# Kernel optimization log

Measured on AMD Instinct MI355X. Metric: run time of the kernel, lower is better.

Reference implementation:

```python
import jax, jax.numpy as jnp
import numpy as np

EPS = 1e-6

def _quant_per_token(x):
    # dynamic per-token symmetric int8 quantization (simulated in float)
    s = jnp.max(jnp.abs(x), axis=-1, keepdims=True) / 127.0  # [T,1]
    q = jnp.clip(jnp.round(x / s), -127.0, 127.0)
    return q, s

def _quant_weight(W):
    # per-output-channel symmetric int8 weight quantization (W: [out,in])
    s = jnp.max(jnp.abs(W), axis=1, keepdims=True) / 127.0  # [out,1]
    q = jnp.round(W / s)
    return q, s

def _w8a8(qx, sx, W, b):
    # int8xint8 GEMM with per-token act scale and per-channel weight scale, fp out
    qw, sw = _quant_weight(W)
    return (qx @ qw.T) * (sx * sw.T) + b

def _rmsnorm_bias(x, w, b, eps=EPS):
    # RMSNormGeneral: x * rsqrt(mean(x^2)+eps) * w + b (no mean subtraction)
    var = jnp.mean(x * x, axis=-1, keepdims=True)
    return x * jax.lax.rsqrt(var + eps) * w + b

def setup_inputs() -> dict:
    key = jax.random.key(0)
    ks = jax.random.split(key, 16)
    E, H, F = 1280, 20, 5120
    B, S = 16, 1024
    T = B * S
    d = {
        'hidden': jax.random.normal(ks[0], (T, E), jnp.float32),
        'ln1_w': jax.random.uniform(ks[1], (E,), jnp.float32, 0.5, 1.5),
        'ln1_b': jax.random.normal(ks[2], (E,), jnp.float32) * 0.02,
        'ln2_w': jax.random.uniform(ks[3], (E,), jnp.float32, 0.5, 1.5),
        'ln2_b': jax.random.normal(ks[4], (E,), jnp.float32) * 0.02,
        'W_qkv': jax.random.normal(ks[5], (3 * E, E), jnp.float32) * 0.02,
        'b_qkv': jax.random.normal(ks[6], (3 * E,), jnp.float32) * 0.02,
        'W_out': jax.random.normal(ks[7], (E, E), jnp.float32) * 0.02,
        'b_out': jax.random.normal(ks[8], (E,), jnp.float32) * 0.02,
        'W_fc1': jax.random.normal(ks[9], (F, E), jnp.float32) * 0.02,
        'b_fc1': jax.random.normal(ks[10], (F,), jnp.float32) * 0.02,
        'W_fc2': jax.random.normal(ks[11], (E, F), jnp.float32) * 0.02,
        'b_fc2': jax.random.normal(ks[12], (E,), jnp.float32) * 0.02,
        'bsz': B,
        'seqlen': S,
    }
    return d

def reference(hidden, ln1_w, ln1_b, ln2_w, ln2_b, W_qkv, b_qkv, W_out, b_out,
              W_fc1, b_fc1, W_fc2, b_fc2, bsz, seqlen):
    E = hidden.shape[-1]
    H = 20
    hd = E // H

    # --- self-attention block ---
    residual = hidden
    y = _rmsnorm_bias(hidden, ln1_w, ln1_b)
    qx, sx = _quant_per_token(y)
    qkv = _w8a8(qx, sx, W_qkv, b_qkv)                      # [T, 3E]
    q, k, v = jnp.split(qkv, 3, axis=-1)
    q = q.reshape(bsz, seqlen, H, hd)
    k = k.reshape(bsz, seqlen, H, hd)
    v = v.reshape(bsz, seqlen, H, hd)
    scale = 1.0 / np.sqrt(hd)
    scores = jnp.einsum('bqhd,bkhd->bhqk', q, k) * scale   # non-causal
    probs = jax.nn.softmax(scores, axis=-1)
    attn = jnp.einsum('bhqk,bkhd->bqhd', probs, v).reshape(bsz * seqlen, E)
    qa, sa = _quant_per_token(attn)
    o = _w8a8(qa, sa, W_out, b_out)
    hidden = residual + o

    # --- MLP block ---
    residual = hidden
    y = _rmsnorm_bias(hidden, ln2_w, ln2_b)
    qx, sx = _quant_per_token(y)
    f1 = _w8a8(qx, sx, W_fc1, b_fc1)                       # [T, F]
    g = jax.nn.gelu(f1, approximate=False)                 # fused gelu_and_quant
    qg, sg = _quant_per_token(g)
    f2 = _w8a8(qg, sg, W_fc2, b_fc2)
    return residual + f2
```

## Files before the change

### kernel.cpp

```cpp
#include <hip/hip_runtime.h>
#include <hip/hip_bf16.h>
#include <stdint.h>

#define E_DIM 1280
#define F_DIM 5120
#define T_DIM 16384
#define B_SZ  16
#define S_LEN 1024
#define NH    20

typedef int v4i __attribute__((ext_vector_type(4)));
typedef __attribute__((ext_vector_type(8))) short v8s;
typedef __attribute__((ext_vector_type(4))) float v4f;

__device__ __forceinline__ float wred_sum(float v) {
#pragma unroll
  for (int m = 32; m > 0; m >>= 1) v += __shfl_xor(v, m, 64);
  return v;
}
__device__ __forceinline__ float wred_max(float v) {
#pragma unroll
  for (int m = 32; m > 0; m >>= 1) v = fmaxf(v, __shfl_xor(v, m, 64));
  return v;
}
__device__ __forceinline__ void gload_lds16(const void* g, void* l) {
  __builtin_amdgcn_global_load_lds((const __attribute__((address_space(1))) void*)g,
                                   (__attribute__((address_space(3))) void*)l, 16, 0, 0);
}

__global__ __launch_bounds__(256) void wquant_kernel(
    const float* __restrict__ W, int8_t* __restrict__ qw, float* __restrict__ sw, int K) {
  __shared__ float red[4];
  const int row = blockIdx.x;
  const int tid = threadIdx.x;
  const float* wr = W + (size_t)row * K;
  float amax = 0.f;
  for (int c = tid; c < K; c += 256) amax = fmaxf(amax, fabsf(wr[c]));
  amax = wred_max(amax);
  if ((tid & 63) == 0) red[tid >> 6] = amax;
  __syncthreads();
  amax = fmaxf(fmaxf(red[0], red[1]), fmaxf(red[2], red[3]));
  float sc = amax * (1.0f / 127.0f);
  if (tid == 0) sw[row] = sc;
  for (int c = tid; c < K; c += 256) {
    float qv = rintf(wr[c] / sc);
    qw[(size_t)row * K + c] = (int8_t)qv;
  }
}

__global__ __launch_bounds__(256) void rms_quant_kernel(
    const float* __restrict__ x, const float* __restrict__ w, const float* __restrict__ b,
    int8_t* __restrict__ q, float* __restrict__ s) {
  __shared__ float red[4];
  const int row = blockIdx.x;
  const int tid = threadIdx.x;
  const float* xr = x + (size_t)row * E_DIM;
  float vals[5];
  float ss = 0.f;
#pragma unroll
  for (int i = 0; i < 5; ++i) {
    float v = xr[tid + i * 256];
    vals[i] = v; ss += v * v;
  }
  ss = wred_sum(ss);
  if ((tid & 63) == 0) red[tid >> 6] = ss;
  __syncthreads();
  ss = red[0] + red[1] + red[2] + red[3];
  float rstd = rsqrtf(ss * (1.0f / E_DIM) + 1e-6f);
  float y[5]; float amax = 0.f;
#pragma unroll
  for (int i = 0; i < 5; ++i) {
    int c = tid + i * 256;
    float v = vals[i] * rstd * w[c] + b[c];
    y[i] = v;
    amax = fmaxf(amax, fabsf(v));
  }
  amax = wred_max(amax);
  __syncthreads();
  if ((tid & 63) == 0) red[tid >> 6] = amax;
  __syncthreads();
  amax = fmaxf(fmaxf(red[0], red[1]), fmaxf(red[2], red[3]));
  float sc = amax * (1.0f / 127.0f);
  if (tid == 0) s[row] = sc;
#pragma unroll
  for (int i = 0; i < 5; ++i) {
    int c = tid + i * 256;
    float qv = rintf(y[i] / sc);
    qv = fminf(fmaxf(qv, -127.f), 127.f);
    q[(size_t)row * E_DIM + c] = (int8_t)qv;
  }
}

__global__ __launch_bounds__(256) void row_quant_bf_kernel(
    const __hip_bfloat16* __restrict__ x, int8_t* __restrict__ q, float* __restrict__ s) {
  __shared__ float red[4];
  const int row = blockIdx.x;
  const int tid = threadIdx.x;
  const __hip_bfloat16* xr = x + (size_t)row * E_DIM;
  float vals[5]; float amax = 0.f;
#pragma unroll
  for (int i = 0; i < 5; ++i) {
    float v = __bfloat162float(xr[tid + i * 256]);
    vals[i] = v;
    amax = fmaxf(amax, fabsf(v));
  }
  amax = wred_max(amax);
  if ((tid & 63) == 0) red[tid >> 6] = amax;
  __syncthreads();
  amax = fmaxf(fmaxf(red[0], red[1]), fmaxf(red[2], red[3]));
  float sc = amax * (1.0f / 127.0f);
  if (tid == 0) s[row] = sc;
#pragma unroll
  for (int i = 0; i < 5; ++i) {
    int c = tid + i * 256;
    float qv = rintf(vals[i] / sc);
    qv = fminf(fmaxf(qv, -127.f), 127.f);
    q[(size_t)row * E_DIM + c] = (int8_t)qv;
  }
}

__global__ __launch_bounds__(256) void gelu_quant_kernel(
    const __hip_bfloat16* __restrict__ f1, int8_t* __restrict__ q, float* __restrict__ s) {
  __shared__ float red[4];
  const int row = blockIdx.x;
  const int tid = threadIdx.x;
  const __hip_bfloat16* xr = f1 + (size_t)row * F_DIM;
  float g[20]; float amax = 0.f;
#pragma unroll
  for (int i = 0; i < 20; ++i) {
    float v = __bfloat162float(xr[tid + i * 256]);
    float gv = 0.5f * v * (1.0f + erff(v * 0.70710678118654752440f));
    g[i] = gv;
    amax = fmaxf(amax, fabsf(gv));
  }
  amax = wred_max(amax);
  if ((tid & 63) == 0) red[tid >> 6] = amax;
  __syncthreads();
  amax = fmaxf(fmaxf(red[0], red[1]), fmaxf(red[2], red[3]));
  float sc = amax * (1.0f / 127.0f);
  if (tid == 0) s[row] = sc;
  int8_t* qr = q + (size_t)row * (2 * F_DIM);
#pragma unroll
  for (int i = 0; i < 20; ++i) {
    int c = tid + i * 256;
    float qv = rintf(g[i] / sc);
    qv = fminf(fmaxf(qv, -127.f), 127.f);
    qr[c] = (int8_t)qv;
  }
}

template <int MODE>
__global__ __launch_bounds__(512, 2) void gemm256_i8(
    const int8_t* __restrict__ A, const int8_t* __restrict__ B,
    const float* __restrict__ sx, const float* __restrict__ sw,
    const float* __restrict__ bias, const float* __restrict__ resid,
    void* __restrict__ outp, int M, int N, int K, int lda) {
  __shared__ __align__(16) int8_t As[2][2][256 * 64];
  __shared__ __align__(16) int8_t Bs[2][2][256 * 64];

  const int tid = threadIdx.x;
  const int lane = tid & 63;
  const int wave = tid >> 6;
  const int wm = wave >> 2;
  const int wn = wave & 3;
  const int l16 = lane & 15;
  const int quad = lane >> 4;
  const int choff = (quad ^ ((l16 >> 1) & 3)) << 4;

  const int nwg = gridDim.x;
  const int ntn = N >> 8;
  const int u = (blockIdx.x & 7) * (nwg >> 3) + (blockIdx.x >> 3);
  const int tm = u / ntn, tn = u % ntn;
  const int m0 = tm << 8, n0 = tn << 8;

  const int8_t* A_blk = A + (size_t)m0 * lda;
  const int8_t* B_blk = B + (size_t)n0 * K;

  const int r0 = tid >> 2;
  const int sch = ((tid & 3) ^ ((tid >> 3) & 3)) << 4;

#define STAGE_A(KT, DST)                                                         \
  {                                                                              \
    gload_lds16(A_blk + (size_t)r0 * lda + (size_t)(KT)*64 + sch,                \
                (DST) + tid * 16);                                               \
    gload_lds16(A_blk + (size_t)(r0 + 128) * lda + (size_t)(KT)*64 + sch,        \
                (DST) + 8192 + tid * 16);                                        \
  }
#define STAGE_B(KT, DST)                                                         \
  {                                                                              \
    gload_lds16(B_blk + (size_t)r0 * K + (size_t)(KT)*64 + sch,                  \
                (DST) + tid * 16);                                               \
    gload_lds16(B_blk + (size_t)(r0 + 128) * K + (size_t)(KT)*64 + sch,          \
                (DST) + 8192 + tid * 16);                                        \
  }

  v4i acc[8][4];
#pragma unroll
  for (int i = 0; i < 8; ++i)
#pragma unroll
    for (int j = 0; j < 4; ++j) acc[i][j] = (v4i){0, 0, 0, 0};

  const int nk = K >> 6;
  const int niter = nk >> 1;

  STAGE_A(0, &As[0][0][0]); STAGE_B(0, &Bs[0][0][0]);
  STAGE_A(1, &As[0][1][0]); STAGE_B(1, &Bs[0][1][0]);
  asm volatile("s_waitcnt vmcnt(4)" ::: "memory");
  asm volatile("s_barrier" ::: "memory");

#pragma unroll 1
  for (int i = 0; i < niter - 1; ++i) {
    const int pr = i & 1;
    const int kt2 = 2 * i + 2;
#pragma unroll
    for (int ph = 0; ph < 4; ++ph) {
      const int tt = ph >> 1;
      const int qm = ph & 1;
      const int8_t* At = &As[pr][tt][0];
      const int8_t* Bt = &Bs[pr][tt][0];
      v4i af[4], bf[4];
#pragma unroll
      for (int ii = 0; ii < 4; ++ii)
        af[ii] = *(const v4i*)(At + (wm * 128 + qm * 64 + ii * 16 + l16) * 64 + choff);
#pragma unroll
      for (int jj = 0; jj < 4; ++jj)
        bf[jj] = *(const v4i*)(Bt + (wn * 64 + jj * 16 + l16) * 64 + choff);
      if (qm == 0) {
        STAGE_A(kt2 + tt, &As[pr ^ 1][tt][0]);
      } else {
        STAGE_B(kt2 + tt, &Bs[pr ^ 1][tt][0]);
      }
      asm volatile("s_barrier" ::: "memory");
      __builtin_amdgcn_s_setprio(1);
#pragma unroll
      for (int ii = 0; ii < 4; ++ii)
#pragma unroll
        for (int jj = 0; jj < 4; ++jj)
          acc[qm * 4 + ii][jj] = __builtin_amdgcn_mfma_i32_16x16x64_i8(
              af[ii], bf[jj], acc[qm * 4 + ii][jj], 0, 0, 0);
      __builtin_amdgcn_s_setprio(0);
      if (qm == 1) asm volatile("s_waitcnt vmcnt(4)" ::: "memory");
      asm volatile("s_barrier" ::: "memory");
    }
  }

  {
    const int pr = (niter - 1) & 1;
#pragma unroll
    for (int ph = 0; ph < 4; ++ph) {
      const int tt = ph >> 1;
      const int qm = ph & 1;
      const int8_t* At = &As[pr][tt][0];
      const int8_t* Bt = &Bs[pr][tt][0];
      v4i af[4], bf[4];
#pragma unroll
      for (int ii = 0; ii < 4; ++ii)
        af[ii] = *(const v4i*)(At + (wm * 128 + qm * 64 + ii * 16 + l16) * 64 + choff);
#pragma unroll
      for (int jj = 0; jj < 4; ++jj)
        bf[jj] = *(const v4i*)(Bt + (wn * 64 + jj * 16 + l16) * 64 + choff);
      asm volatile("s_barrier" ::: "memory");
      __builtin_amdgcn_s_setprio(1);
#pragma unroll
      for (int ii = 0; ii < 4; ++ii)
#pragma unroll
        for (int jj = 0; jj < 4; ++jj)
          acc[qm * 4 + ii][jj] = __builtin_amdgcn_mfma_i32_16x16x64_i8(
              af[ii], bf[jj], acc[qm * 4 + ii][jj], 0, 0, 0);
      __builtin_amdgcn_s_setprio(0);
      if (ph == 1) asm volatile("s_waitcnt vmcnt(0)" ::: "memory");
      asm volatile("s_barrier" ::: "memory");
    }
  }
#undef STAGE_A
#undef STAGE_B

  float swv[4], bv[4];
#pragma unroll
  for (int jj = 0; jj < 4; ++jj) {
    int n = n0 + wn * 64 + jj * 16 + l16;
    swv[jj] = sw[n];
    bv[jj] = bias[n];
  }
#pragma unroll
  for (int mf = 0; mf < 8; ++mf) {
#pragma unroll
    for (int r = 0; r < 4; ++r) {
      int m = m0 + wm * 128 + mf * 16 + quad * 4 + r;
      float sxm = sx[m];
#pragma unroll
      for (int jj = 0; jj < 4; ++jj) {
        int n = n0 + wn * 64 + jj * 16 + l16;
        float v = (float)acc[mf][jj][r] * (sxm * swv[jj]) + bv[jj];
        if constexpr (MODE == 0) {
          ((__hip_bfloat16*)outp)[(size_t)m * N + n] = __float2bfloat16(v);
        } else {
          ((float*)outp)[(size_t)m * N + n] = v + resid[(size_t)m * N + n];
        }
      }
    }
  }
}

template <int MODE>
__global__ __launch_bounds__(256, 2) void gemm128_i8(
    const int8_t* __restrict__ A, const int8_t* __restrict__ B,
    const float* __restrict__ sx, const float* __restrict__ sw,
    const float* __restrict__ bias, const float* __restrict__ resid,
    void* __restrict__ outp, int M, int N, int K, int lda) {
  __shared__ __align__(16) int8_t As[4][128 * 64];
  __shared__ __align__(16) int8_t Bs[4][128 * 64];

  const int tid = threadIdx.x;
  const int lane = tid & 63;
  const int wave = tid >> 6;
  const int wm = wave >> 1;
  const int wn = wave & 1;
  const int l16 = lane & 15;
  const int quad = lane >> 4;
  const int choff = (quad ^ ((l16 >> 1) & 3)) << 4;

  const int nwg = gridDim.x;
  const int ntn = N >> 7;
  const int u = (blockIdx.x & 7) * (nwg >> 3) + (blockIdx.x >> 3);
  const int tm = u / ntn, tn = u % ntn;
  const int m0 = tm << 7, n0 = tn << 7;

  const int8_t* A_blk = A + (size_t)m0 * lda;
  const int8_t* B_blk = B + (size_t)n0 * K;

  const int r0 = tid >> 2;
  const int sch = ((tid & 3) ^ ((tid >> 3) & 3)) << 4;

#define STAGE_A(KT, SLOT)                                                        \
  {                                                                              \
    gload_lds16(A_blk + (size_t)r0 * lda + (size_t)(KT)*64 + sch,                \
                &As[SLOT][tid * 16]);                                            \
    gload_lds16(A_blk + (size_t)(r0 + 64) * lda + (size_t)(KT)*64 + sch,         \
                &As[SLOT][4096 + tid * 16]);                                     \
  }
#define STAGE_B(KT, SLOT)                                                        \
  {                                                                              \
    gload_lds16(B_blk + (size_t)r0 * K + (size_t)(KT)*64 + sch,                  \
                &Bs[SLOT][tid * 16]);                                            \
    gload_lds16(B_blk + (size_t)(r0 + 64) * K + (size_t)(KT)*64 + sch,           \
                &Bs[SLOT][4096 + tid * 16]);                                     \
  }

#define KTILE(SLOT, STAGE_STMT, WAIT_STMT)                                       \
  {                                                                              \
    const int8_t* At = &As[SLOT][0];                                             \
    const int8_t* Bt = &Bs[SLOT][0];                                             \
    v4i af[4], bf[4];                                                            \
    _Pragma("unroll") for (int ii = 0; ii < 4; ++ii)                             \
        af[ii] = *(const v4i*)(At + (wm * 64 + ii * 16 + l16) * 64 + choff);     \
    _Pragma("unroll") for (int jj = 0; jj < 4; ++jj)                             \
        bf[jj] = *(const v4i*)(Bt + (wn * 64 + jj * 16 + l16) * 64 + choff);     \
    STAGE_STMT;                                                                  \
    asm volatile("s_barrier" ::: "memory");                                      \
    __builtin_amdgcn_s_setprio(1);                                               \
    _Pragma("unroll") for (int ii = 0; ii < 4; ++ii)                             \
        _Pragma("unroll") for (int jj = 0; jj < 4; ++jj)                         \
            acc[ii][jj] = __builtin_amdgcn_mfma_i32_16x16x64_i8(                 \
                af[ii], bf[jj], acc[ii][jj], 0, 0, 0);                           \
    __builtin_amdgcn_s_setprio(0);                                               \
    WAIT_STMT;                                                                   \
    asm volatile("s_barrier" ::: "memory");                                      \
  }

  v4i acc[4][4];
#pragma unroll
  for (int i = 0; i < 4; ++i)
#pragma unroll
    for (int j = 0; j < 4; ++j) acc[i][j] = (v4i){0, 0, 0, 0};

  const int nk = K >> 6;

  STAGE_A(0, 0); STAGE_B(0, 0);
  STAGE_A(1, 1); STAGE_B(1, 1);
  STAGE_A(2, 2); STAGE_B(2, 2);
  asm volatile("s_waitcnt vmcnt(8)" ::: "memory");
  asm volatile("s_barrier" ::: "memory");

#pragma unroll 1
  for (int kt = 0; kt < nk - 3; ++kt) {
    const int sl = kt & 3;
    const int s3 = (kt + 3) & 3;
    KTILE(sl, { STAGE_A(kt + 3, s3); STAGE_B(kt + 3, s3); },
          asm volatile("s_waitcnt vmcnt(8)" ::: "memory"));
  }
  KTILE((nk - 3) & 3, ((void)0), asm volatile("s_waitcnt vmcnt(4)" ::: "memory"));
  KTILE((nk - 2) & 3, ((void)0), asm volatile("s_waitcnt vmcnt(0)" ::: "memory"));
  KTILE((nk - 1) & 3, ((void)0), ((void)0));
#undef KTILE
#undef STAGE_A
#undef STAGE_B

  float swv[4], bv[4];
#pragma unroll
  for (int jj = 0; jj < 4; ++jj) {
    int n = n0 + wn * 64 + jj * 16 + l16;
    swv[jj] = sw[n];
    bv[jj] = bias[n];
  }
#pragma unroll
  for (int ii = 0; ii < 4; ++ii) {
#pragma unroll
    for (int r = 0; r < 4; ++r) {
      int m = m0 + wm * 64 + ii * 16 + quad * 4 + r;
      float sxm = sx[m];
#pragma unroll
      for (int jj = 0; jj < 4; ++jj) {
        int n = n0 + wn * 64 + jj * 16 + l16;
        float v = (float)acc[ii][jj][r] * (sxm * swv[jj]) + bv[jj];
        if constexpr (MODE == 0) {
          ((__hip_bfloat16*)outp)[(size_t)m * N + n] = __float2bfloat16(v);
        } else {
          ((float*)outp)[(size_t)m * N + n] = v + resid[(size_t)m * N + n];
        }
      }
    }
  }
}

__global__ __launch_bounds__(256) void vt_kernel(
    const __hip_bfloat16* __restrict__ qkv, __hip_bfloat16* __restrict__ Vt) {
  __shared__ __hip_bfloat16 tile[64][72];
  const int bh = blockIdx.y, kc = blockIdx.x;
  const int b = bh / NH, h = bh % NH;
  const int tid = threadIdx.x;
  const size_t base = ((size_t)b * S_LEN + (size_t)kc * 64) * (3 * E_DIM) + 2 * E_DIM + h * 64;
#pragma unroll
  for (int i = 0; i < 2; ++i) {
    int idx = tid + i * 256;
    int row = idx >> 3, c8 = (idx & 7) * 8;
    *(uint4*)&tile[row][c8] = *(const uint4*)(qkv + base + (size_t)row * (3 * E_DIM) + c8);
  }
  __syncthreads();
#pragma unroll
  for (int i = 0; i < 2; ++i) {
    int idx = tid + i * 256;
    int d = idx >> 3, k8 = (idx & 7) * 8;
    __hip_bfloat16 v[8] __attribute__((aligned(16)));
#pragma unroll
    for (int j = 0; j < 8; ++j) v[j] = tile[k8 + j][d];
    *(uint4*)&Vt[((size_t)bh * 64 + d) * 1024 + (size_t)kc * 64 + k8] = *(uint4*)v;
  }
}

__global__ __launch_bounds__(256) void attn_flash_kernel(
    const __hip_bfloat16* __restrict__ qkv, const __hip_bfloat16* __restrict__ Vt,
    __hip_bfloat16* __restrict__ attn) {
  constexpr int E3 = 3 * E_DIM;
  __shared__ __align__(16) __hip_bfloat16 Ks[128 * 64];
  __shared__ __align__(16) __hip_bfloat16 Vs[64 * 128];
  __shared__ __align__(16) __hip_bfloat16 Ps[4][16 * 128];
  __shared__ float stats[4][16];

  const int tid = threadIdx.x;
  const int lane = tid & 63;
  const int wave = tid >> 6;
  const int l16 = lane & 15;
  const int quad = lane >> 4;
  const int wg = (blockIdx.x & 7) * 640 + (blockIdx.x >> 3);
  const int bh = wg >> 4;
  const int b = bh / NH, h = bh % NH;
  const int q0 = (wg & 15) * 64;
  const size_t base_t = (size_t)b * S_LEN;

  v8s qb0, qb1;
  {
    const __hip_bfloat16* qp =
        qkv + (base_t + q0 + wave * 16 + l16) * (size_t)E3 + h * 64 + quad * 8;
    qb0 = *(const v8s*)qp;
    qb1 = *(const v8s*)(qp + 32);
  }

  const __hip_bfloat16* kgbase = qkv + base_t * E3 + E_DIM + h * 64;
  const __hip_bfloat16* vgbase = Vt + (size_t)bh * 64 * 1024;
  __hip_bfloat16* pw = Ps[wave];

  const __hip_bfloat16* ksrc[4];
  const __hip_bfloat16* vsrc[4];
  int cdst[4];
#pragma unroll
  for (int i = 0; i < 4; ++i) {
    int c = tid + i * 256;
    cdst[i] = c * 16;
    int row = c >> 3, lc = c & 7;
    int gc = lc ^ (row & 7);
    ksrc[i] = kgbase + (size_t)row * E3 + gc * 8;
    int d = c >> 4, lcv = c & 15;
    int gv = lcv ^ (d & 15);
    vsrc[i] = vgbase + (size_t)d * 1024 + gv * 8;
  }

#pragma unroll
  for (int i = 0; i < 4; ++i) gload_lds16(ksrc[i], (char*)Ks + cdst[i]);
#pragma unroll
  for (int i = 0; i < 4; ++i) gload_lds16(vsrc[i], (char*)Vs + cdst[i]);
  __syncthreads();

  constexpr float CEXP = 0.18033688011112042f;
  float m_prev = -3.0e38f;
  float mc = m_prev * CEXP;
  float lsum = 0.f;
  v4f oc[4];
#pragma unroll
  for (int dt = 0; dt < 4; ++dt) oc[dt] = (v4f){0.f, 0.f, 0.f, 0.f};

#pragma unroll 1
  for (int t = 0; t < 8; ++t) {
    v4i kreg[4], vreg[4];
    if (t < 7) {
#pragma unroll
      for (int i = 0; i < 4; ++i)
        kreg[i] = *(const v4i*)(ksrc[i] + (size_t)(t + 1) * 128 * E3);
#pragma unroll
      for (int i = 0; i < 4; ++i)
        vreg[i] = *(const v4i*)(vsrc[i] + (size_t)(t + 1) * 128);
    }

    v4f accT[8];
    __builtin_amdgcn_s_setprio(1);
#pragma unroll
    for (int nt = 0; nt < 8; ++nt) {
      int row = nt * 16 + l16;
      const char* kr = (const char*)Ks + row * 128;
      v8s ak0 = *(const v8s*)(kr + ((quad ^ (row & 7)) * 16));
      v8s ak1 = *(const v8s*)(kr + (((quad + 4) ^ (row & 7)) * 16));
      v4f z = {0.f, 0.f, 0.f, 0.f};
      z = __builtin_amdgcn_mfma_f32_16x16x32_bf16(ak0, qb0, z, 0, 0, 0);
      accT[nt] = __builtin_amdgcn_mfma_f32_16x16x32_bf16(ak1, qb1, accT[nt] = z, 0, 0, 0);
    }
    __builtin_amdgcn_s_setprio(0);

    float mt = -3.0e38f;
#pragma unroll
    for (int nt = 0; nt < 8; ++nt)
      mt = fmaxf(mt, fmaxf(fmaxf(accT[nt][0], accT[nt][1]),
                           fmaxf(accT[nt][2], accT[nt][3])));
    mt = fmaxf(mt, __shfl_xor(mt, 16, 64));
    mt = fmaxf(mt, __shfl_xor(mt, 32, 64));
    if (__any(mt > m_prev + 48.0f)) {
      float m_new = fmaxf(m_prev, mt);
      float mcn = m_new * CEXP;
      float alpha = exp2f(m_prev * CEXP - mcn);
      m_prev = m_new;
      mc = mcn;
      lsum *= alpha;
      if (quad == 0) stats[wave][l16] = alpha;
      v4f a4 = *(v4f*)&stats[wave][quad * 4];
#pragma unroll
      for (int dt = 0; dt < 4; ++dt)
#pragma unroll
        for (int r = 0; r < 4; ++r) oc[dt][r] *= a4[r];
    }
    float ts = 0.f;
#pragma unroll
    for (int nt = 0; nt < 8; ++nt)
#pragma unroll
      for (int r = 0; r < 4; ++r) {
        float e = exp2f(fmaf(accT[nt][r], CEXP, -mc));
        accT[nt][r] = e;
        ts += e;
      }
    lsum += ts;
#pragma unroll
    for (int nt = 0; nt < 8; ++nt) {
      __hip_bfloat16 pk[4] __attribute__((aligned(8)));
#pragma unroll
      for (int r = 0; r < 4; ++r) pk[r] = __float2bfloat16(accT[nt][r]);
      int lcq = 2 * nt + (quad >> 1);
      *(uint2*)((char*)pw + l16 * 256 + ((lcq ^ l16) * 16) + (quad & 1) * 8) = *(uint2*)pk;
    }
    __builtin_amdgcn_s_setprio(1);
#pragma unroll
    for (int ks = 0; ks < 4; ++ks) {
      int pch = (ks * 4 + quad) ^ l16;
      v8s ap = *(const v8s*)((char*)pw + l16 * 256 + pch * 16);
#pragma unroll
      for (int dt = 0; dt < 4; ++dt) {
        int d = dt * 16 + l16;
        v8s bv = *(const v8s*)((char*)Vs + d * 256 + (((ks * 4 + quad) ^ l16) * 16));
        oc[dt] = __builtin_amdgcn_mfma_f32_16x16x32_bf16(ap, bv, oc[dt], 0, 0, 0);
      }
    }
    __builtin_amdgcn_s_setprio(0);

    __syncthreads();
    if (t < 7) {
#pragma unroll
      for (int i = 0; i < 4; ++i) *(v4i*)((char*)Ks + cdst[i]) = kreg[i];
#pragma unroll
      for (int i = 0; i < 4; ++i) *(v4i*)((char*)Vs + cdst[i]) = vreg[i];
    }
    __syncthreads();
  }

  lsum += __shfl_xor(lsum, 16, 64);
  lsum += __shfl_xor(lsum, 32, 64);
  if (quad == 0) stats[wave][l16] = lsum;
  v4f l4 = *(v4f*)&stats[wave][quad * 4];
  float inv[4];
#pragma unroll
  for (int r = 0; r < 4; ++r) inv[r] = 1.0f / l4[r];
#pragma unroll
  for (int dt = 0; dt < 4; ++dt)
#pragma unroll
    for (int r = 0; r < 4; ++r) {
      int tok = q0 + wave * 16 + quad * 4 + r;
      attn[(base_t + tok) * (size_t)E_DIM + h * 64 + dt * 16 + l16] =
          __float2bfloat16(oc[dt][r] * inv[r]);
    }
}

extern "C" void kernel_launch(void* const* d_in, const int* in_sizes, int n_in,
                              void* d_out, int out_size, void* d_ws, size_t ws_size,
                              hipStream_t stream) {
  const float* hidden = (const float*)d_in[0];
  const float* ln1_w = (const float*)d_in[1];
  const float* ln1_b = (const float*)d_in[2];
  const float* ln2_w = (const float*)d_in[3];
  const float* ln2_b = (const float*)d_in[4];
  const float* W_qkv = (const float*)d_in[5];
  const float* b_qkv = (const float*)d_in[6];
  const float* W_out = (const float*)d_in[7];
  const float* b_out = (const float*)d_in[8];
  const float* W_fc1 = (const float*)d_in[9];
  const float* b_fc1 = (const float*)d_in[10];
  const float* W_fc2 = (const float*)d_in[11];
  const float* b_fc2 = (const float*)d_in[12];

  char* ws = (char*)d_ws;
  size_t off = 0;
  auto alloc = [&](size_t bytes) {
    void* p = ws + off;
    off += (bytes + 255) & ~(size_t)255;
    return p;
  };
  int8_t* qw_qkv = (int8_t*)alloc((size_t)3 * E_DIM * E_DIM);
  int8_t* qw_out = (int8_t*)alloc((size_t)E_DIM * E_DIM);
  int8_t* qw_fc1 = (int8_t*)alloc((size_t)F_DIM * E_DIM);
  int8_t* qw_fc2 = (int8_t*)alloc((size_t)E_DIM * F_DIM);
  float* sw_qkv = (float*)alloc((size_t)3 * E_DIM * 4);
  float* sw_out = (float*)alloc((size_t)E_DIM * 4);
  float* sw_fc1 = (float*)alloc((size_t)F_DIM * 4);
  float* sw_fc2 = (float*)alloc((size_t)E_DIM * 4);
  float* sx1 = (float*)alloc((size_t)T_DIM * 4);
  float* sa  = (float*)alloc((size_t)T_DIM * 4);
  float* sx2 = (float*)alloc((size_t)T_DIM * 4);
  float* sg  = (float*)alloc((size_t)T_DIM * 4);
  int8_t* qx = (int8_t*)alloc((size_t)T_DIM * E_DIM);
  char* R = (char*)alloc((size_t)T_DIM * 3 * E_DIM * 2 +
                         (size_t)T_DIM * E_DIM * 4);
  __hip_bfloat16* qkv_bf = (__hip_bfloat16*)R;
  __hip_bfloat16* attn_bf = (__hip_bfloat16*)(R + (size_t)T_DIM * 3 * E_DIM * 2);
  __hip_bfloat16* Vt = (__hip_bfloat16*)(R + (size_t)T_DIM * 3 * E_DIM * 2 +
                                         (size_t)T_DIM * E_DIM * 2);
  __hip_bfloat16* f1_bf = (__hip_bfloat16*)R;
  int8_t* qg = (int8_t*)R;
  float* hidden2 = (float*)d_out;

  wquant_kernel<<<3 * E_DIM, 256, 0, stream>>>(W_qkv, qw_qkv, sw_qkv, E_DIM);
  wquant_kernel<<<E_DIM, 256, 0, stream>>>(W_out, qw_out, sw_out, E_DIM);
  wquant_kernel<<<F_DIM, 256, 0, stream>>>(W_fc1, qw_fc1, sw_fc1, E_DIM);
  wquant_kernel<<<E_DIM, 256, 0, stream>>>(W_fc2, qw_fc2, sw_fc2, F_DIM);
  rms_quant_kernel<<<T_DIM, 256, 0, stream>>>(hidden, ln1_w, ln1_b, qx, sx1);
  gemm256_i8<0><<<(T_DIM / 256) * (3 * E_DIM / 256), 512, 0, stream>>>(
      qx, qw_qkv, sx1, sw_qkv, b_qkv, nullptr, qkv_bf, T_DIM, 3 * E_DIM, E_DIM, E_DIM);
  vt_kernel<<<dim3(S_LEN / 64, B_SZ * NH), 256, 0, stream>>>(qkv_bf, Vt);
  attn_flash_kernel<<<(S_LEN / 64) * B_SZ * NH, 256, 0, stream>>>(qkv_bf, Vt, attn_bf);
  row_quant_bf_kernel<<<T_DIM, 256, 0, stream>>>(attn_bf, qx, sa);
  gemm128_i8<1><<<(T_DIM / 128) * (E_DIM / 128), 256, 0, stream>>>(
      qx, qw_out, sa, sw_out, b_out, hidden, hidden2, T_DIM, E_DIM, E_DIM, E_DIM);
  rms_quant_kernel<<<T_DIM, 256, 0, stream>>>(hidden2, ln2_w, ln2_b, qx, sx2);
  gemm256_i8<0><<<(T_DIM / 256) * (F_DIM / 256), 512, 0, stream>>>(
      qx, qw_fc1, sx2, sw_fc1, b_fc1, nullptr, f1_bf, T_DIM, F_DIM, E_DIM, E_DIM);
  gelu_quant_kernel<<<T_DIM, 256, 0, stream>>>(f1_bf, qg, sg);
  gemm128_i8<1><<<(T_DIM / 128) * (E_DIM / 128), 256, 0, stream>>>(
      qg, qw_fc2, sg, sw_fc2, b_fc2, hidden2, (float*)d_out, T_DIM, E_DIM, F_DIM, 2 * F_DIM);
}
```

Before: 1.045 ms.

## Drop register prefetch in flash attention, load K/V directly to LDS each tile

Removes the register-staged prefetch of the next K/V tile and instead issues direct global-to-LDS loads at the start of each iteration between barriers. It also precomputes the swizzled LDS offsets outside the loop and adds a launch bound of 3 blocks per CU. The aim is to cut VGPR pressure so more waves fit per CU and hide latency through occupancy. The cost is that loads are no longer overlapped with compute inside a block, so each tile now waits on memory latency.

```diff
diff --git a/kernel.cpp b/kernel.cpp
--- a/kernel.cpp
+++ b/kernel.cpp
@@ -448,7 +448,7 @@
   }
 }
 
-__global__ __launch_bounds__(256) void attn_flash_kernel(
+__global__ __launch_bounds__(256, 3) void attn_flash_kernel(
     const __hip_bfloat16* __restrict__ qkv, const __hip_bfloat16* __restrict__ Vt,
     __hip_bfloat16* __restrict__ attn) {
   constexpr int E3 = 3 * E_DIM;
@@ -476,30 +476,44 @@
     qb1 = *(const v8s*)(qp + 32);
   }
 
-  const __hip_bfloat16* kgbase = qkv + base_t * E3 + E_DIM + h * 64;
-  const __hip_bfloat16* vgbase = Vt + (size_t)bh * 64 * 1024;
   __hip_bfloat16* pw = Ps[wave];
 
-  const __hip_bfloat16* ksrc[4];
-  const __hip_bfloat16* vsrc[4];
+  const __hip_bfloat16* kp[4];
+  const __hip_bfloat16* vp[4];
   int cdst[4];
-#pragma unroll
-  for (int i = 0; i < 4; ++i) {
-    int c = tid + i * 256;
-    cdst[i] = c * 16;
-    int row = c >> 3, lc = c & 7;
-    int gc = lc ^ (row & 7);
-    ksrc[i] = kgbase + (size_t)row * E3 + gc * 8;
-    int d = c >> 4, lcv = c & 15;
-    int gv = lcv ^ (d & 15);
-    vsrc[i] = vgbase + (size_t)d * 1024 + gv * 8;
-  }
-
-#pragma unroll
-  for (int i = 0; i < 4; ++i) gload_lds16(ksrc[i], (char*)Ks + cdst[i]);
-#pragma unroll
-  for (int i = 0; i < 4; ++i) gload_lds16(vsrc[i], (char*)Vs + cdst[i]);
-  __syncthreads();
+  {
+    const __hip_bfloat16* kgbase = qkv + base_t * E3 + E_DIM + h * 64;
+    const __hip_bfloat16* vgbase = Vt + (size_t)bh * 64 * 1024;
+#pragma unroll
+    for (int i = 0; i < 4; ++i) {
+      int c = tid + i * 256;
+      cdst[i] = c * 16;
+      int row = c >> 3, lc = c & 7;
+      int gc = lc ^ (row & 7);
+      kp[i] = kgbase + (size_t)row * E3 + gc * 8;
+      int d = c >> 4, lcv = c & 15;
+      int gv = lcv ^ (d & 15);
+      vp[i] = vgbase + (size_t)d * 1024 + gv * 8;
+    }
+  }
+
+  const int cho0 = (quad ^ (l16 & 7)) << 4;
+  const int cho1 = ((quad + 4) ^ (l16 & 7)) << 4;
+  const char* krbase = (const char*)Ks + l16 * 128;
+  char* pwr[8];
+#pragma unroll
+  for (int nt = 0; nt < 8; ++nt) {
+    int lcq = 2 * nt + (quad >> 1);
+    pwr[nt] = (char*)pw + l16 * 256 + ((lcq ^ l16) * 16) + (quad & 1) * 8;
+  }
+  const char* pvp[4];
+  int vvo[4];
+#pragma unroll
+  for (int ks = 0; ks < 4; ++ks) {
+    int pch16 = (((ks * 4 + quad) ^ l16) << 4);
+    pvp[ks] = (char*)pw + l16 * 256 + pch16;
+    vvo[ks] = l16 * 256 + pch16;
+  }
 
   constexpr float CEXP = 0.18033688011112042f;
   float m_prev = -3.0e38f;
@@ -511,24 +525,22 @@
 
 #pragma unroll 1
   for (int t = 0; t < 8; ++t) {
-    v4i kreg[4], vreg[4];
-    if (t < 7) {
-#pragma unroll
-      for (int i = 0; i < 4; ++i)
-        kreg[i] = *(const v4i*)(ksrc[i] + (size_t)(t + 1) * 128 * E3);
-#pragma unroll
-      for (int i = 0; i < 4; ++i)
-        vreg[i] = *(const v4i*)(vsrc[i] + (size_t)(t + 1) * 128);
-    }
+    __syncthreads();
+#pragma unroll
+    for (int i = 0; i < 4; ++i) gload_lds16(kp[i], (char*)Ks + cdst[i]);
+#pragma unroll
+    for (int i = 0; i < 4; ++i) gload_lds16(vp[i], (char*)Vs + cdst[i]);
+#pragma unroll
+    for (int i = 0; i < 4; ++i) { kp[i] += (size_t)128 * E3; vp[i] += 128; }
+    __syncthreads();
 
     v4f accT[8];
     __builtin_amdgcn_s_setprio(1);
 #pragma unroll
     for (int nt = 0; nt < 8; ++nt) {
-      int row = nt * 16 + l16;
-      const char* kr = (const char*)Ks + row * 128;
-      v8s ak0 = *(const v8s*)(kr + ((quad ^ (row & 7)) * 16));
-      v8s ak1 = *(const v8s*)(kr + (((quad + 4) ^ (row & 7)) * 16));
+      const char* kr = krbase + nt * 2048;
+      v8s ak0 = *(const v8s*)(kr + cho0);
+      v8s ak1 = *(const v8s*)(kr + cho1);
       v4f z = {0.f, 0.f, 0.f, 0.f};
       z = __builtin_amdgcn_mfma_f32_16x16x32_bf16(ak0, qb0, z, 0, 0, 0);
       accT[nt] = __builtin_amdgcn_mfma_f32_16x16x32_bf16(ak1, qb1, accT[nt] = z, 0, 0, 0);
@@ -571,31 +583,19 @@
       __hip_bfloat16 pk[4] __attribute__((aligned(8)));
 #pragma unroll
       for (int r = 0; r < 4; ++r) pk[r] = __float2bfloat16(accT[nt][r]);
-      int lcq = 2 * nt + (quad >> 1);
-      *(uint2*)((char*)pw + l16 * 256 + ((lcq ^ l16) * 16) + (quad & 1) * 8) = *(uint2*)pk;
+      *(uint2*)pwr[nt] = *(uint2*)pk;
     }
     __builtin_amdgcn_s_setprio(1);
 #pragma unroll
     for (int ks = 0; ks < 4; ++ks) {
-      int pch = (ks * 4 + quad) ^ l16;
-      v8s ap = *(const v8s*)((char*)pw + l16 * 256 + pch * 16);
+      v8s ap = *(const v8s*)pvp[ks];
 #pragma unroll
       for (int dt = 0; dt < 4; ++dt) {
-        int d = dt * 16 + l16;
-        v8s bv = *(const v8s*)((char*)Vs + d * 256 + (((ks * 4 + quad) ^ l16) * 16));
+        v8s bv = *(const v8s*)((char*)Vs + vvo[ks] + dt * 4096);
         oc[dt] = __builtin_amdgcn_mfma_f32_16x16x32_bf16(ap, bv, oc[dt], 0, 0, 0);
       }
     }
     __builtin_amdgcn_s_setprio(0);
-
-    __syncthreads();
-    if (t < 7) {
-#pragma unroll
-      for (int i = 0; i < 4; ++i) *(v4i*)((char*)Ks + cdst[i]) = kreg[i];
-#pragma unroll
-      for (int i = 0; i < 4; ++i) *(v4i*)((char*)Vs + cdst[i]) = vreg[i];
-    }
-    __syncthreads();
   }
 
   lsum += __shfl_xor(lsum, 16, 64);
```

Measured after the change: 1.058 ms. Within noise of the previous version (+1.2%).
